# Performance work log

Hardware: AMD Instinct MI355X
Metric: run time of the kernel (lower is better)

The kernel has to match this reference:

```python
import jax, jax.numpy as jnp
import numpy as np

N = 100000      # nodes
E = 1600000     # directed edges (before self-loops)
DIN = 128       # input feature dim
HID = 32        # per-head hidden dim
HEADS = 4
D1 = HID * HEADS  # 128, concat width
NG = 64         # graphs in batch
NEG_SLOPE = 0.2 # PyG GATConv leaky_relu slope


def setup_inputs() -> dict:
    key = jax.random.key(0)
    ks = jax.random.split(key, 16)
    s = 0.05
    x = jax.random.normal(ks[0], (N, DIN), dtype=jnp.float32)
    edge_index = jax.random.randint(ks[1], (2, E), 0, N, dtype=jnp.int32)
    batch = jnp.sort(jax.random.randint(ks[2], (N,), 0, NG, dtype=jnp.int32))
    # GATConv 1: in=DIN, out=HID, heads=HEADS, concat=True
    W1 = jax.random.normal(ks[3], (D1, DIN), dtype=jnp.float32) * s
    a1s = jax.random.normal(ks[4], (HEADS, HID), dtype=jnp.float32) * s
    a1d = jax.random.normal(ks[5], (HEADS, HID), dtype=jnp.float32) * s
    b1 = jnp.zeros((D1,), jnp.float32)
    # GATConv 2: in=D1, out=HID, heads=HEADS, concat=True
    W2 = jax.random.normal(ks[6], (D1, D1), dtype=jnp.float32) * s
    a2s = jax.random.normal(ks[7], (HEADS, HID), dtype=jnp.float32) * s
    a2d = jax.random.normal(ks[8], (HEADS, HID), dtype=jnp.float32) * s
    b2 = jnp.zeros((D1,), jnp.float32)
    # GATConv 3: in=D1, out=HID, heads=HEADS, concat=False (mean over heads)
    W3 = jax.random.normal(ks[9], (D1, D1), dtype=jnp.float32) * s
    a3s = jax.random.normal(ks[10], (HEADS, HID), dtype=jnp.float32) * s
    a3d = jax.random.normal(ks[11], (HEADS, HID), dtype=jnp.float32) * s
    b3 = jnp.zeros((HID,), jnp.float32)
    lin_w = jax.random.normal(ks[12], (1, HID), dtype=jnp.float32) * s
    lin_b = jnp.zeros((1,), jnp.float32)
    return {"x": x, "edge_index": edge_index, "batch": batch,
            "W1": W1, "a1s": a1s, "a1d": a1d, "b1": b1,
            "W2": W2, "a2s": a2s, "a2d": a2d, "b2": b2,
            "W3": W3, "a3s": a3s, "a3d": a3d, "b3": b3,
            "lin_w": lin_w, "lin_b": lin_b}


def _gat_conv(x, ei, W, att_src, att_dst, bias, concat):
    """PyG GATConv (no edge features, self-loops already in ei)."""
    n = x.shape[0]
    h = (x @ W.T).reshape(n, HEADS, HID)          # [N, H, C]
    src, dst = ei[0], ei[1]
    a_src = jnp.einsum('nhc,hc->nh', h, att_src)  # [N, H]
    a_dst = jnp.einsum('nhc,hc->nh', h, att_dst)
    e = jax.nn.leaky_relu(a_src[src] + a_dst[dst], NEG_SLOPE)  # [Etot, H]
    # segment softmax over incoming edges of each dst node
    e_max = jax.ops.segment_max(e, dst, num_segments=n)
    ex = jnp.exp(e - e_max[dst])
    denom = jax.ops.segment_sum(ex, dst, num_segments=n)
    alpha = ex / denom[dst]                        # [Etot, H]
    out = jax.ops.segment_sum(h[src] * alpha[:, :, None], dst, num_segments=n)
    if concat:
        out = out.reshape(n, HEADS * HID)
    else:
        out = out.mean(axis=1)
    return out + bias


def reference(x, edge_index, batch, W1, a1s, a1d, b1, W2, a2s, a2d, b2,
              W3, a3s, a3d, b3, lin_w, lin_b):
    loops = jnp.arange(N, dtype=edge_index.dtype)
    ei = jnp.concatenate([edge_index, jnp.stack([loops, loops])], axis=1)
    h = jax.nn.elu(_gat_conv(x, ei, W1, a1s, a1d, b1, True))
    h = jax.nn.elu(_gat_conv(h, ei, W2, a2s, a2d, b2, True))
    h = jax.nn.elu(_gat_conv(h, ei, W3, a3s, a3d, b3, False))
    h = h @ lin_w.T + lin_b                        # [N, 1]
    counts = jax.ops.segment_sum(jnp.ones((N,), h.dtype), batch, num_segments=NG)
    pooled = jax.ops.segment_sum(h, batch, num_segments=NG) / counts[:, None]
    return pooled.squeeze()                        # [NG]
```

## Files before the change

kernel.cpp:

```cpp
#include <hip/hip_runtime.h>
#include <hip/hip_fp16.h>
#include <math.h>

#define D1 128
#define NEG 0.2f
#define NODE_SHIFT 9
#define BIN_NODES 512
#define MAXBIN 256

typedef short v8s __attribute__((ext_vector_type(8)));
typedef float v4f __attribute__((ext_vector_type(4)));

__device__ __forceinline__ float lrelu(float v){ return v > 0.f ? v : NEG * v; }
__device__ __forceinline__ float elu_f(float v){ return v > 0.f ? v : __expf(v) - 1.f; }

__device__ __forceinline__ unsigned short bf16s(float f){
    unsigned u = __float_as_uint(f);
    return (unsigned short)((u + 0x7fffu + ((u >> 16) & 1u)) >> 16);
}
__device__ __forceinline__ float bf2f(unsigned short s){
    return __uint_as_float(((unsigned)s) << 16);
}
__device__ __forceinline__ unsigned f2h2(float a, float b){
    return ((unsigned)__half_as_ushort(__float2half_rn(b)) << 16) |
           (unsigned)__half_as_ushort(__float2half_rn(a));
}
__device__ __forceinline__ float2 h2f2(unsigned u){
    float lo = __half2float(__ushort_as_half((unsigned short)(u & 0xffffu)));
    float hi = __half2float(__ushort_as_half((unsigned short)(u >> 16)));
    return make_float2(lo, hi);
}


__global__ __launch_bounds__(256) void kb_hist(const int* __restrict__ ei,
                                               int* __restrict__ binCnt,
                                               int n_edges, int etot, int nbin){
    __shared__ int h[MAXBIN];
    for (int i = threadIdx.x; i < nbin; i += 256) h[i] = 0;
    __syncthreads();
    int stride = gridDim.x * 256;
    for (int e = blockIdx.x * 256 + threadIdx.x; e < etot; e += stride){
        int dst = (e < n_edges) ? ei[n_edges + e] : (e - n_edges);
        atomicAdd(&h[dst >> NODE_SHIFT], 1);
    }
    __syncthreads();
    for (int i = threadIdx.x; i < nbin; i += 256)
        if (h[i]) atomicAdd(&binCnt[i], h[i]);
}

__global__ void kb_scan(const int* __restrict__ binCnt, int* __restrict__ binStart,
                        int* __restrict__ binCursor, int nbin,
                        int* __restrict__ rowptr, int n_nodes, int etot){
    if (threadIdx.x == 0){
        int run = 0;
        for (int b = 0; b < nbin; b++){
            binStart[b] = run; binCursor[b] = run; run += binCnt[b];
        }
        binStart[nbin] = run;
        rowptr[n_nodes] = etot;
    }
}

__global__ __launch_bounds__(256) void kb_scatter(const int* __restrict__ ei,
                                                  int* __restrict__ binCursor,
                                                  uint2* __restrict__ staged,
                                                  int n_edges, int etot, int nbin){
    __shared__ int cnt[MAXBIN];
    __shared__ int base[MAXBIN];
    int e0 = blockIdx.x * 4096;
    for (int i = threadIdx.x; i < nbin; i += 256) cnt[i] = 0;
    __syncthreads();
    #pragma unroll 4
    for (int r = 0; r < 16; r++){
        int e = e0 + r * 256 + threadIdx.x;
        if (e < etot){
            int dst = (e < n_edges) ? ei[n_edges + e] : (e - n_edges);
            atomicAdd(&cnt[dst >> NODE_SHIFT], 1);
        }
    }
    __syncthreads();
    for (int i = threadIdx.x; i < nbin; i += 256){
        base[i] = cnt[i] ? atomicAdd(&binCursor[i], cnt[i]) : 0;
        cnt[i] = 0;
    }
    __syncthreads();
    #pragma unroll 4
    for (int r = 0; r < 16; r++){
        int e = e0 + r * 256 + threadIdx.x;
        if (e < etot){
            int src, dst;
            if (e < n_edges){ src = ei[e]; dst = ei[n_edges + e]; }
            else            { src = dst = e - n_edges; }
            int b = dst >> NODE_SHIFT;
            int p = base[b] + atomicAdd(&cnt[b], 1);
            staged[p] = make_uint2((unsigned)src, (unsigned)dst);
        }
    }
}

__global__ __launch_bounds__(512) void kb_final(const uint2* __restrict__ staged,
                                                const int* __restrict__ binStart,
                                                int* __restrict__ rowptr,
                                                int* __restrict__ eidx, int n_nodes){
    __shared__ int deg[BIN_NODES];
    __shared__ int cur[BIN_NODES];
    int b = blockIdx.x;
    int nbase = b << NODE_SHIFT;
    int s0 = binStart[b], s1 = binStart[b + 1];
    deg[threadIdx.x] = 0;
    __syncthreads();
    for (int i = s0 + threadIdx.x; i < s1; i += 512)
        atomicAdd(&deg[staged[i].y & (BIN_NODES - 1)], 1);
    __syncthreads();
    int v = deg[threadIdx.x];
    cur[threadIdx.x] = v;
    __syncthreads();
    for (int off = 1; off < BIN_NODES; off <<= 1){
        int t = (threadIdx.x >= off) ? cur[threadIdx.x - off] : 0;
        __syncthreads();
        cur[threadIdx.x] += t;
        __syncthreads();
    }
    int excl = cur[threadIdx.x] - v;
    int node = nbase + threadIdx.x;
    if (node < n_nodes) rowptr[node] = s0 + excl;
    cur[threadIdx.x] = s0 + excl;
    __syncthreads();
    for (int i = s0 + threadIdx.x; i < s1; i += 512){
        uint2 pr = staged[i];
        int p = atomicAdd(&cur[pr.y & (BIN_NODES - 1)], 1);
        eidx[p] = (int)pr.x;
    }
}


__global__ void k_prepw(const float* __restrict__ W1, const float* __restrict__ W2,
                        const float* __restrict__ W3, unsigned short* __restrict__ Bp){
    int t = blockIdx.x * 256 + threadIdx.x;
    if (t >= 49152) return;
    int w = t >> 14;
    int r = t & 16383;
    int k = r >> 7, j = r & 127;
    const float* W = (w == 0) ? W1 : (w == 1) ? W2 : W3;
    float val = W[j * 128 + k];
    unsigned short hi = bf16s(val);
    unsigned short lo = bf16s(val - bf2f(hi));
    int idx = (k >> 3) * 1024 + j * 8 + (k & 7);
    Bp[w * 32768 + idx] = hi;
    Bp[w * 32768 + 16384 + idx] = lo;
}


__global__ void k_split(const float* __restrict__ X, unsigned short* __restrict__ Xhi,
                        unsigned short* __restrict__ Xlo, int nquads){
    int t = blockIdx.x * 256 + threadIdx.x;
    if (t >= nquads) return;
    float4 v = ((const float4*)X)[t];
    ushort4 hi, lo;
    hi.x = bf16s(v.x); lo.x = bf16s(v.x - bf2f(hi.x));
    hi.y = bf16s(v.y); lo.y = bf16s(v.y - bf2f(hi.y));
    hi.z = bf16s(v.z); lo.z = bf16s(v.z - bf2f(hi.z));
    hi.w = bf16s(v.w); lo.w = bf16s(v.w - bf2f(hi.w));
    ((ushort4*)Xhi)[t] = hi;
    ((ushort4*)Xlo)[t] = lo;
}


__global__ __launch_bounds__(256, 4) void k_mgemm(
        const unsigned short* __restrict__ Xhi, const unsigned short* __restrict__ Xlo,
        const unsigned short* __restrict__ Bp,
        const float* __restrict__ aw_s, const float* __restrict__ aw_d,
        unsigned short* __restrict__ Hh,
        float* __restrict__ asrc, float* __restrict__ adst, int n_rows){
    __shared__ unsigned short Bs[16384];
    int lane = threadIdx.x & 63;
    int wv   = threadIdx.x >> 6;
    int li = lane & 15, quad = lane >> 4;
    int r0 = blockIdx.x * 128 + wv * 32;

    int row0 = r0 + li;
    int row1 = r0 + 16 + li;
    int rc0 = row0 < n_rows ? row0 : 0;
    int rc1 = row1 < n_rows ? row1 : 0;

    v4f acc[2][8];
    #pragma unroll
    for (int m = 0; m < 2; m++)
        #pragma unroll
        for (int t = 0; t < 8; t++)
            acc[m][t] = (v4f){0.f, 0.f, 0.f, 0.f};

    #pragma unroll
    for (int g = 0; g < 2; g++){
        if (g) __syncthreads();
        #pragma unroll
        for (int i = 0; i < 4; i++){
            int idx = threadIdx.x + i * 256;
            ((float4*)Bs)[idx]          = ((const float4*)(Bp + g * 8192))[idx];
            ((float4*)(Bs + 8192))[idx] = ((const float4*)(Bp + 16384 + g * 8192))[idx];
        }
        __syncthreads();
        #pragma unroll
        for (int ks2 = 0; ks2 < 2; ks2++){
            int ks = g * 2 + ks2;
            int koff = ks * 32 + quad * 8;
            v8s ah0 = *(const v8s*)(Xhi + (size_t)rc0 * 128 + koff);
            v8s al0 = *(const v8s*)(Xlo + (size_t)rc0 * 128 + koff);
            v8s ah1 = *(const v8s*)(Xhi + (size_t)rc1 * 128 + koff);
            v8s al1 = *(const v8s*)(Xlo + (size_t)rc1 * 128 + koff);
            #pragma unroll
            for (int t = 0; t < 8; t++){
                int bo = ks2 * 4096 + quad * 1024 + (t * 16 + li) * 8;
                v8s bh = *(const v8s*)(Bs + bo);
                v8s bl = *(const v8s*)(Bs + 8192 + bo);
                acc[0][t] = __builtin_amdgcn_mfma_f32_16x16x32_bf16(ah0, bh, acc[0][t], 0, 0, 0);
                acc[0][t] = __builtin_amdgcn_mfma_f32_16x16x32_bf16(ah0, bl, acc[0][t], 0, 0, 0);
                acc[0][t] = __builtin_amdgcn_mfma_f32_16x16x32_bf16(al0, bh, acc[0][t], 0, 0, 0);
                acc[1][t] = __builtin_amdgcn_mfma_f32_16x16x32_bf16(ah1, bh, acc[1][t], 0, 0, 0);
                acc[1][t] = __builtin_amdgcn_mfma_f32_16x16x32_bf16(ah1, bl, acc[1][t], 0, 0, 0);
                acc[1][t] = __builtin_amdgcn_mfma_f32_16x16x32_bf16(al1, bh, acc[1][t], 0, 0, 0);
            }
        }
    }

    #pragma unroll
    for (int m = 0; m < 2; m++){
        #pragma unroll
        for (int t = 0; t < 8; t++){
            #pragma unroll
            for (int r = 0; r < 4; r++){
                float v  = acc[m][t][r];
                float vo = __shfl_xor(v, 1);
                if (!(li & 1)){
                    int row = r0 + m * 16 + quad * 4 + r;
                    if (row < n_rows)
                        *(unsigned*)(Hh + (size_t)row * 128 + t * 16 + li) = f2h2(v, vo);
                }
            }
        }
    }

    float as8[8], ad8[8];
    #pragma unroll
    for (int t = 0; t < 8; t++){
        as8[t] = aw_s[t * 16 + li];
        ad8[t] = aw_d[t * 16 + li];
    }
    #pragma unroll
    for (int m = 0; m < 2; m++){
        #pragma unroll
        for (int r = 0; r < 4; r++){
            float sp[4], dp[4];
            #pragma unroll
            for (int h = 0; h < 4; h++){
                sp[h] = acc[m][2*h][r] * as8[2*h] + acc[m][2*h+1][r] * as8[2*h+1];
                dp[h] = acc[m][2*h][r] * ad8[2*h] + acc[m][2*h+1][r] * ad8[2*h+1];
            }
            #pragma unroll
            for (int off = 1; off < 16; off <<= 1){
                #pragma unroll
                for (int h = 0; h < 4; h++){
                    sp[h] += __shfl_xor(sp[h], off);
                    dp[h] += __shfl_xor(dp[h], off);
                }
            }
            if (li == 0){
                int row = r0 + m * 16 + quad * 4 + r;
                if (row < n_rows){
                    ((float4*)asrc)[row] = make_float4(sp[0], sp[1], sp[2], sp[3]);
                    ((float4*)adst)[row] = make_float4(dp[0], dp[1], dp[2], dp[3]);
                }
            }
        }
    }
}


template<int MEAN>
__global__ __launch_bounds__(256) void k_aggr(
        const unsigned* __restrict__ Hh,
        const float* __restrict__ asrc, const float* __restrict__ adst,
        const int* __restrict__ rowptr, const int* __restrict__ eidx,
        const float* __restrict__ bias,
        unsigned short* __restrict__ Oh, unsigned short* __restrict__ Ol,
        float* __restrict__ Of, int n_nodes){
    int lane = threadIdx.x & 63;
    int wid  = threadIdx.x >> 6;
    int n = blockIdx.x * 4 + wid;
    if (n >= n_nodes) return;
    int row0 = rowptr[n];
    int deg  = rowptr[n + 1] - row0;
    const int* ep = eidx + row0;
    unsigned hd = (unsigned)(lane >> 4);
    unsigned ul = (unsigned)lane;
    float adh = adst[(unsigned)n * 4u + hd];

    float accx = 0.f, accy = 0.f, den = 0.f;
    int i = 0;
    for (; i + 8 <= deg; i += 8){
        unsigned s[8];
        #pragma unroll
        for (int j = 0; j < 8; j++) s[j] = (unsigned)ep[i + j];
        float a[8];
        unsigned hw[8];
        #pragma unroll
        for (int j = 0; j < 8; j++){
            a[j]  = asrc[s[j] * 4u + hd];
            hw[j] = Hh[s[j] * 64u + ul];
        }
        #pragma unroll
        for (int j = 0; j < 8; j++){
            float w = __expf(lrelu(a[j] + adh));
            float2 hv = h2f2(hw[j]);
            den  += w;
            accx += w * hv.x;
            accy += w * hv.y;
        }
    }
    for (; i < deg; i++){
        unsigned s = (unsigned)ep[i];
        float w = __expf(lrelu(asrc[s * 4u + hd] + adh));
        float2 hv = h2f2(Hh[s * 64u + ul]);
        den  += w;
        accx += w * hv.x;
        accy += w * hv.y;
    }
    float rdh = 1.f / den;
    accx *= rdh; accy *= rdh;

    int c = lane * 2;
    if (!MEAN){
        float ox = elu_f(accx + bias[c]);
        float oy = elu_f(accy + bias[c + 1]);
        unsigned short hx = bf16s(ox), hy = bf16s(oy);
        unsigned short lx = bf16s(ox - bf2f(hx)), ly = bf16s(oy - bf2f(hy));
        *(ushort2*)(Oh + (size_t)n * 128 + c) = make_ushort2(hx, hy);
        *(ushort2*)(Ol + (size_t)n * 128 + c) = make_ushort2(lx, ly);
    } else {
        float sx = accx, sy = accy;
        sx += __shfl_xor(sx, 16); sy += __shfl_xor(sy, 16);
        sx += __shfl_xor(sx, 32); sy += __shfl_xor(sy, 32);
        if (lane < 16){
            int cc = lane * 2;
            float ox = elu_f(sx * 0.25f + bias[cc]);
            float oy = elu_f(sy * 0.25f + bias[cc + 1]);
            *(float2*)(Of + (size_t)n * 32 + cc) = make_float2(ox, oy);
        }
    }
}


__global__ void k_readout(const float* __restrict__ H3, const int* __restrict__ batch,
                          const float* __restrict__ lw, const float* __restrict__ lb,
                          float* __restrict__ pool, float* __restrict__ cnt, int n_nodes){
    __shared__ float pl[64];
    __shared__ float cl[64];
    if (threadIdx.x < 64){ pl[threadIdx.x] = 0.f; cl[threadIdx.x] = 0.f; }
    __syncthreads();
    int n = blockIdx.x * 256 + threadIdx.x;
    if (n < n_nodes){
        const float4* hp = (const float4*)(H3 + (size_t)n * 32);
        const float4* wp = (const float4*)lw;
        float y = 0.f;
        #pragma unroll
        for (int i = 0; i < 8; i++){
            float4 h4 = hp[i], w4 = wp[i];
            y += h4.x * w4.x + h4.y * w4.y + h4.z * w4.z + h4.w * w4.w;
        }
        y += lb[0];
        int b = batch[n];
        atomicAdd(&pl[b], y);
        atomicAdd(&cl[b], 1.f);
    }
    __syncthreads();
    if (threadIdx.x < 64 && cl[threadIdx.x] != 0.f){
        atomicAdd(&pool[threadIdx.x], pl[threadIdx.x]);
        atomicAdd(&cnt[threadIdx.x], cl[threadIdx.x]);
    }
}

__global__ void k_final(const float* __restrict__ pool, const float* __restrict__ cnt,
                        float* __restrict__ out){
    int g = threadIdx.x;
    if (g < 64) out[g] = (cnt[g] > 0.f) ? pool[g] / cnt[g] : 0.f;
}


extern "C" void kernel_launch(void* const* d_in, const int* in_sizes, int n_in,
                              void* d_out, int out_size, void* d_ws, size_t ws_size,
                              hipStream_t stream){
    const float* x   = (const float*)d_in[0];
    const int*   ei  = (const int*)  d_in[1];
    const int*   bat = (const int*)  d_in[2];
    const float* W1  = (const float*)d_in[3];
    const float* a1s = (const float*)d_in[4];
    const float* a1d = (const float*)d_in[5];
    const float* b1  = (const float*)d_in[6];
    const float* W2  = (const float*)d_in[7];
    const float* a2s = (const float*)d_in[8];
    const float* a2d = (const float*)d_in[9];
    const float* b2  = (const float*)d_in[10];
    const float* W3  = (const float*)d_in[11];
    const float* a3s = (const float*)d_in[12];
    const float* a3d = (const float*)d_in[13];
    const float* b3  = (const float*)d_in[14];
    const float* lw  = (const float*)d_in[15];
    const float* lb  = (const float*)d_in[16];
    (void)n_in; (void)out_size; (void)ws_size;

    const int n_nodes = in_sizes[0] / D1;
    const int n_edges = in_sizes[1] / 2;
    const int etot    = n_edges + n_nodes;
    const int nbin    = (n_nodes + BIN_NODES - 1) >> NODE_SHIFT;

    char* p = (char*)d_ws;
    size_t off = 0;
    auto alloc = [&](size_t bytes) -> char* {
        char* r = p + off;
        off = (off + bytes + 511) & ~(size_t)511;
        return r;
    };
    unsigned short* Hh   = (unsigned short*)alloc((size_t)n_nodes * 128 * 2);
    unsigned short* Xhi  = (unsigned short*)alloc((size_t)n_nodes * 128 * 2);
    unsigned short* Xlo  = (unsigned short*)alloc((size_t)n_nodes * 128 * 2);
    float*          asrc = (float*)alloc((size_t)n_nodes * 4 * 4);
    float*          adst = (float*)alloc((size_t)n_nodes * 4 * 4);
    unsigned short* Bp   = (unsigned short*)alloc(3 * 32768 * 2);
    int*   rowptr  = (int*)alloc((size_t)(n_nodes + 1) * 4);
    int*   eidx    = (int*)alloc((size_t)etot * 4);
    uint2* staged  = (uint2*)alloc((size_t)etot * 8);
    int*   binCnt  = (int*)alloc(MAXBIN * 4);
    int*   binStart= (int*)alloc((MAXBIN + 1) * 4);
    int*   binCur  = (int*)alloc(MAXBIN * 4);
    float* pool    = (float*)alloc(64 * 4);
    float* cnt     = (float*)alloc(64 * 4);
    float* h3      = (float*)Xhi;

    hipMemsetAsync(binCnt, 0, MAXBIN * 4, stream);
    hipMemsetAsync(pool, 0, 64 * 4, stream);
    hipMemsetAsync(cnt, 0, 64 * 4, stream);

    k_prepw<<<192, 256, 0, stream>>>(W1, W2, W3, Bp);

    int cb = (etot + 4095) / 4096;
    kb_hist<<<cb, 256, 0, stream>>>(ei, binCnt, n_edges, etot, nbin);
    kb_scan<<<1, 64, 0, stream>>>(binCnt, binStart, binCur, nbin, rowptr, n_nodes, etot);
    kb_scatter<<<cb, 256, 0, stream>>>(ei, binCur, staged, n_edges, etot, nbin);
    kb_final<<<nbin, 512, 0, stream>>>(staged, binStart, rowptr, eidx, n_nodes);

    int nquads = n_nodes * 32;
    k_split<<<(nquads + 255) / 256, 256, 0, stream>>>(x, Xhi, Xlo, nquads);

    int mb = (n_nodes + 127) / 128;
    int rb = (n_nodes + 3) / 4;

    k_mgemm<<<mb, 256, 0, stream>>>(Xhi, Xlo, Bp, a1s, a1d, Hh, asrc, adst, n_nodes);
    k_aggr<0><<<rb, 256, 0, stream>>>((const unsigned*)Hh, asrc, adst, rowptr, eidx,
                                      b1, Xhi, Xlo, nullptr, n_nodes);
    k_mgemm<<<mb, 256, 0, stream>>>(Xhi, Xlo, Bp + 32768, a2s, a2d, Hh, asrc, adst, n_nodes);
    k_aggr<0><<<rb, 256, 0, stream>>>((const unsigned*)Hh, asrc, adst, rowptr, eidx,
                                      b2, Xhi, Xlo, nullptr, n_nodes);
    k_mgemm<<<mb, 256, 0, stream>>>(Xhi, Xlo, Bp + 65536, a3s, a3d, Hh, asrc, adst, n_nodes);
    k_aggr<1><<<rb, 256, 0, stream>>>((const unsigned*)Hh, asrc, adst, rowptr, eidx,
                                      b3, nullptr, nullptr, h3, n_nodes);

    int ob = (n_nodes + 255) / 256;
    k_readout<<<ob, 256, 0, stream>>>(h3, bat, lw, lb, pool, cnt, n_nodes);
    k_final<<<1, 64, 0, stream>>>(pool, cnt, (float*)d_out);
}
```

Baseline: 556.4 us.

## Fuse fp32 input split into first GEMM, stage full weights, share attention exps

Removes the separate k_split kernel by having the first GEMM load fp32 inputs and split them into bf16 hi/lo in registers. The GEMM now preloads all A fragments and stages the whole 64KB hi/lo weight matrix in dynamic shared memory with a single barrier, where it previously used two staged halves. In the aggregation kernel, each lane computes one edge-head attention weight, which is then broadcast via shuffles, so the exp/leaky-relu work and asrc loads are no longer repeated across the 16 lanes of each head. The 64KB shared allocation and the extra register arrays may lower GEMM occupancy.

```diff
diff --git a/kernel.cpp b/kernel.cpp
--- a/kernel.cpp
+++ b/kernel.cpp
@@ -29,6 +29,14 @@
     float lo = __half2float(__ushort_as_half((unsigned short)(u & 0xffffu)));
     float hi = __half2float(__ushort_as_half((unsigned short)(u >> 16)));
     return make_float2(lo, hi);
+}
+__device__ __forceinline__ void split8(const float* f, v8s& hi, v8s& lo){
+    #pragma unroll
+    for (int i = 0; i < 8; i++){
+        unsigned short h = bf16s(f[i]);
+        ((short*)&hi)[i] = (short)h;
+        ((short*)&lo)[i] = (short)bf16s(f[i] - bf2f(h));
+    }
 }
 
 
@@ -151,31 +159,18 @@
 }
 
 
-__global__ void k_split(const float* __restrict__ X, unsigned short* __restrict__ Xhi,
-                        unsigned short* __restrict__ Xlo, int nquads){
-    int t = blockIdx.x * 256 + threadIdx.x;
-    if (t >= nquads) return;
-    float4 v = ((const float4*)X)[t];
-    ushort4 hi, lo;
-    hi.x = bf16s(v.x); lo.x = bf16s(v.x - bf2f(hi.x));
-    hi.y = bf16s(v.y); lo.y = bf16s(v.y - bf2f(hi.y));
-    hi.z = bf16s(v.z); lo.z = bf16s(v.z - bf2f(hi.z));
-    hi.w = bf16s(v.w); lo.w = bf16s(v.w - bf2f(hi.w));
-    ((ushort4*)Xhi)[t] = hi;
-    ((ushort4*)Xlo)[t] = lo;
-}
-
-
-__global__ __launch_bounds__(256, 4) void k_mgemm(
+template<int FP32SRC>
+__global__ __launch_bounds__(256) void k_mgemm(
+        const float* __restrict__ Xf,
         const unsigned short* __restrict__ Xhi, const unsigned short* __restrict__ Xlo,
         const unsigned short* __restrict__ Bp,
         const float* __restrict__ aw_s, const float* __restrict__ aw_d,
         unsigned short* __restrict__ Hh,
         float* __restrict__ asrc, float* __restrict__ adst, int n_rows){
-    __shared__ unsigned short Bs[16384];
+    extern __shared__ unsigned short Bs[];
     int lane = threadIdx.x & 63;
-    int wv   = threadIdx.x >> 6;
     int li = lane & 15, quad = lane >> 4;
+    int wv = threadIdx.x >> 6;
     int r0 = blockIdx.x * 128 + wv * 32;
 
     int row0 = r0 + li;
@@ -183,6 +178,33 @@
     int rc0 = row0 < n_rows ? row0 : 0;
     int rc1 = row1 < n_rows ? row1 : 0;
 
+    v8s ah0[4], al0[4], ah1[4], al1[4];
+    #pragma unroll
+    for (int ks = 0; ks < 4; ks++){
+        int koff = ks * 32 + quad * 8;
+        if (FP32SRC){
+            float f0[8], f1[8];
+            *(float4*)&f0[0] = *(const float4*)(Xf + (size_t)rc0 * 128 + koff);
+            *(float4*)&f0[4] = *(const float4*)(Xf + (size_t)rc0 * 128 + koff + 4);
+            *(float4*)&f1[0] = *(const float4*)(Xf + (size_t)rc1 * 128 + koff);
+            *(float4*)&f1[4] = *(const float4*)(Xf + (size_t)rc1 * 128 + koff + 4);
+            split8(f0, ah0[ks], al0[ks]);
+            split8(f1, ah1[ks], al1[ks]);
+        } else {
+            ah0[ks] = *(const v8s*)(Xhi + (size_t)rc0 * 128 + koff);
+            al0[ks] = *(const v8s*)(Xlo + (size_t)rc0 * 128 + koff);
+            ah1[ks] = *(const v8s*)(Xhi + (size_t)rc1 * 128 + koff);
+            al1[ks] = *(const v8s*)(Xlo + (size_t)rc1 * 128 + koff);
+        }
+    }
+
+    #pragma unroll
+    for (int i = 0; i < 16; i++){
+        int idx = threadIdx.x + i * 256;
+        ((float4*)Bs)[idx] = ((const float4*)Bp)[idx];
+    }
+    __syncthreads();
+
     v4f acc[2][8];
     #pragma unroll
     for (int m = 0; m < 2; m++)
@@ -191,35 +213,18 @@
             acc[m][t] = (v4f){0.f, 0.f, 0.f, 0.f};
 
     #pragma unroll
-    for (int g = 0; g < 2; g++){
-        if (g) __syncthreads();
-        #pragma unroll
-        for (int i = 0; i < 4; i++){
-            int idx = threadIdx.x + i * 256;
-            ((float4*)Bs)[idx]          = ((const float4*)(Bp + g * 8192))[idx];
-            ((float4*)(Bs + 8192))[idx] = ((const float4*)(Bp + 16384 + g * 8192))[idx];
-        }
-        __syncthreads();
-        #pragma unroll
-        for (int ks2 = 0; ks2 < 2; ks2++){
-            int ks = g * 2 + ks2;
-            int koff = ks * 32 + quad * 8;
-            v8s ah0 = *(const v8s*)(Xhi + (size_t)rc0 * 128 + koff);
-            v8s al0 = *(const v8s*)(Xlo + (size_t)rc0 * 128 + koff);
-            v8s ah1 = *(const v8s*)(Xhi + (size_t)rc1 * 128 + koff);
-            v8s al1 = *(const v8s*)(Xlo + (size_t)rc1 * 128 + koff);
-            #pragma unroll
-            for (int t = 0; t < 8; t++){
-                int bo = ks2 * 4096 + quad * 1024 + (t * 16 + li) * 8;
-                v8s bh = *(const v8s*)(Bs + bo);
-                v8s bl = *(const v8s*)(Bs + 8192 + bo);
-                acc[0][t] = __builtin_amdgcn_mfma_f32_16x16x32_bf16(ah0, bh, acc[0][t], 0, 0, 0);
-                acc[0][t] = __builtin_amdgcn_mfma_f32_16x16x32_bf16(ah0, bl, acc[0][t], 0, 0, 0);
-                acc[0][t] = __builtin_amdgcn_mfma_f32_16x16x32_bf16(al0, bh, acc[0][t], 0, 0, 0);
-                acc[1][t] = __builtin_amdgcn_mfma_f32_16x16x32_bf16(ah1, bh, acc[1][t], 0, 0, 0);
-                acc[1][t] = __builtin_amdgcn_mfma_f32_16x16x32_bf16(ah1, bl, acc[1][t], 0, 0, 0);
-                acc[1][t] = __builtin_amdgcn_mfma_f32_16x16x32_bf16(al1, bh, acc[1][t], 0, 0, 0);
-            }
+    for (int ks = 0; ks < 4; ks++){
+        #pragma unroll
+        for (int t = 0; t < 8; t++){
+            int bo = (ks * 4 + quad) * 1024 + (t * 16 + li) * 8;
+            v8s bh = *(const v8s*)(Bs + bo);
+            v8s bl = *(const v8s*)(Bs + 16384 + bo);
+            acc[0][t] = __builtin_amdgcn_mfma_f32_16x16x32_bf16(ah0[ks], bh, acc[0][t], 0, 0, 0);
+            acc[0][t] = __builtin_amdgcn_mfma_f32_16x16x32_bf16(ah0[ks], bl, acc[0][t], 0, 0, 0);
+            acc[0][t] = __builtin_amdgcn_mfma_f32_16x16x32_bf16(al0[ks], bh, acc[0][t], 0, 0, 0);
+            acc[1][t] = __builtin_amdgcn_mfma_f32_16x16x32_bf16(ah1[ks], bh, acc[1][t], 0, 0, 0);
+            acc[1][t] = __builtin_amdgcn_mfma_f32_16x16x32_bf16(ah1[ks], bl, acc[1][t], 0, 0, 0);
+            acc[1][t] = __builtin_amdgcn_mfma_f32_16x16x32_bf16(al1[ks], bh, acc[1][t], 0, 0, 0);
         }
     }
 
@@ -293,7 +298,11 @@
     const int* ep = eidx + row0;
     unsigned hd = (unsigned)(lane >> 4);
     unsigned ul = (unsigned)lane;
-    float adh = adst[(unsigned)n * 4u + hd];
+    float4 ad = ((const float4*)adst)[n];
+    float adh = hd == 0 ? ad.x : hd == 1 ? ad.y : hd == 2 ? ad.z : ad.w;
+    unsigned wh = (ul >> 3) & 3;
+    float adw = wh == 0 ? ad.x : wh == 1 ? ad.y : wh == 2 ? ad.z : ad.w;
+    int wsrc = (int)(hd * 8);
 
     float accx = 0.f, accy = 0.f, den = 0.f;
     int i = 0;
@@ -301,20 +310,18 @@
         unsigned s[8];
         #pragma unroll
         for (int j = 0; j < 8; j++) s[j] = (unsigned)ep[i + j];
-        float a[8];
+        float aW = asrc[s[ul & 7] * 4u + wh];
+        float w = __expf(lrelu(aW + adw));
         unsigned hw[8];
         #pragma unroll
+        for (int j = 0; j < 8; j++) hw[j] = Hh[s[j] * 64u + ul];
+        #pragma unroll
         for (int j = 0; j < 8; j++){
-            a[j]  = asrc[s[j] * 4u + hd];
-            hw[j] = Hh[s[j] * 64u + ul];
-        }
-        #pragma unroll
-        for (int j = 0; j < 8; j++){
-            float w = __expf(lrelu(a[j] + adh));
+            float wj = __shfl(w, wsrc + j);
             float2 hv = h2f2(hw[j]);
-            den  += w;
-            accx += w * hv.x;
-            accy += w * hv.y;
+            den  += wj;
+            accx += wj * hv.x;
+            accy += wj * hv.y;
         }
     }
     for (; i < deg; i++){
@@ -448,19 +455,19 @@
     kb_scatter<<<cb, 256, 0, stream>>>(ei, binCur, staged, n_edges, etot, nbin);
     kb_final<<<nbin, 512, 0, stream>>>(staged, binStart, rowptr, eidx, n_nodes);
 
-    int nquads = n_nodes * 32;
-    k_split<<<(nquads + 255) / 256, 256, 0, stream>>>(x, Xhi, Xlo, nquads);
-
     int mb = (n_nodes + 127) / 128;
     int rb = (n_nodes + 3) / 4;
 
-    k_mgemm<<<mb, 256, 0, stream>>>(Xhi, Xlo, Bp, a1s, a1d, Hh, asrc, adst, n_nodes);
+    k_mgemm<1><<<mb, 256, 65536, stream>>>(x, nullptr, nullptr, Bp,
+                                           a1s, a1d, Hh, asrc, adst, n_nodes);
     k_aggr<0><<<rb, 256, 0, stream>>>((const unsigned*)Hh, asrc, adst, rowptr, eidx,
                                       b1, Xhi, Xlo, nullptr, n_nodes);
-    k_mgemm<<<mb, 256, 0, stream>>>(Xhi, Xlo, Bp + 32768, a2s, a2d, Hh, asrc, adst, n_nodes);
+    k_mgemm<0><<<mb, 256, 65536, stream>>>(nullptr, Xhi, Xlo, Bp + 32768,
+                                           a2s, a2d, Hh, asrc, adst, n_nodes);
     k_aggr<0><<<rb, 256, 0, stream>>>((const unsigned*)Hh, asrc, adst, rowptr, eidx,
                                       b2, Xhi, Xlo, nullptr, n_nodes);
-    k_mgemm<<<mb, 256, 0, stream>>>(Xhi, Xlo, Bp + 65536, a3s, a3d, Hh, asrc, adst, n_nodes);
+    k_mgemm<0><<<mb, 256, 65536, stream>>>(nullptr, Xhi, Xlo, Bp + 65536,
+                                           a3s, a3d, Hh, asrc, adst, n_nodes);
     k_aggr<1><<<rb, 256, 0, stream>>>((const unsigned*)Hh, asrc, adst, rowptr, eidx,
                                       b3, nullptr, nullptr, h3, n_nodes);
 
```

New measurement: 572.8 us. 2.9% more time.
